# Kernel tuning notes

Hardware: AMD Instinct MI355X
Metric: run time of the kernel (lower is better)

## Reference

```python
import jax, jax.numpy as jnp
import numpy as np

B, S, HID, NH = 2, 2048, 1024, 16
HD = HID // NH  # head_dim = 64


def setup_inputs() -> dict:
    key = jax.random.key(0)
    ks = jax.random.split(key, 9)
    init = 0.02
    return {
        "x": jax.random.normal(ks[0], (B, S, HID), dtype=jnp.float32),
        "Wq": jax.random.normal(ks[1], (HID, HID), dtype=jnp.float32) * init,
        "bq": jnp.zeros((HID,), dtype=jnp.float32),
        "Wk": jax.random.normal(ks[2], (HID, HID), dtype=jnp.float32) * init,
        "bk": jnp.zeros((HID,), dtype=jnp.float32),
        "Wv": jax.random.normal(ks[3], (HID, HID), dtype=jnp.float32) * init,
        "bv": jnp.zeros((HID,), dtype=jnp.float32),
        "Wo": jax.random.normal(ks[4], (HID, HID), dtype=jnp.float32) * init,
        "bo": jnp.zeros((HID,), dtype=jnp.float32),
    }


def _split_heads(t):
    # [B, S, HID] -> [B, NH, S, HD]
    return t.reshape(B, S, NH, HD).transpose(0, 2, 1, 3)


def reference(x, Wq, bq, Wk, bk, Wv, bv, Wo, bo):
    q = _split_heads(x @ Wq.T + bq)
    k = _split_heads(x @ Wk.T + bk)
    v = _split_heads(x @ Wv.T + bv)

    # Faithful to source: scores = QK^T / (head_dim ** -0.5) == QK^T * sqrt(head_dim)
    inv_scale = jnp.asarray(HD ** (-0.5), dtype=x.dtype)
    scores = jnp.einsum("bhqd,bhkd->bhqk", q, k) / inv_scale

    causal_mask = jnp.triu(jnp.ones((S, S), dtype=bool), k=1)  # True above diagonal
    scores = jnp.where(causal_mask, jnp.asarray(-jnp.inf, dtype=scores.dtype), scores)
    attn = jax.nn.softmax(scores, axis=-1)  # dropout = identity (eval mode)

    ctx = jnp.einsum("bhqk,bhkd->bhqd", attn, v)
    ctx = ctx.transpose(0, 2, 1, 3).reshape(B, S, HID)
    out = ctx @ Wo.T + bo  # out_layer Linear; dropout = identity
    return out, attn
```

## Files before the change

### kernel.cpp

```cpp
#include <hip/hip_runtime.h>
#include <hip/hip_bf16.h>

#define BB   2
#define SS   2048
#define HID  1024
#define NH   16
#define HD   64
#define NEGS -30000.0f

typedef __bf16 bf16x8 __attribute__((ext_vector_type(8)));
typedef float  f32x4  __attribute__((ext_vector_type(4)));

static __device__ __forceinline__ f32x4 mfma_bf16(bf16x8 a, bf16x8 b, f32x4 c) {
    return __builtin_amdgcn_mfma_f32_16x16x32_bf16(a, b, c, 0, 0, 0);
}

static __device__ __forceinline__ void split_bf16(float f, __bf16* hp, __bf16* lp) {
    __bf16 h = (__bf16)f;
    *hp = h;
    *lp = (__bf16)(f - (float)h);
}

static __device__ __forceinline__ float clampf(float v, float lo, float hi) {
    return fminf(fmaxf(v, lo), hi);
}

__global__ __launch_bounds__(256) void qkv_kernel(
    const float* __restrict__ x,
    const float* __restrict__ Wq, const float* __restrict__ bq,
    const float* __restrict__ Wk, const float* __restrict__ bk,
    const float* __restrict__ Wv, const float* __restrict__ bv,
    __bf16* __restrict__ qh, __bf16* __restrict__ ql,
    __bf16* __restrict__ kh, __bf16* __restrict__ kl,
    __bf16* __restrict__ vt)
{
    __shared__ __align__(16) __bf16 Ash[64][40], Asl[64][40];
    __shared__ __align__(16) __bf16 Bsh[64][40], Bsl[64][40];
    __shared__ __align__(16) __bf16 Vts[64][72];

    const int nt = blockIdx.x;
    const int mt = blockIdx.y;
    const int stream_id = nt >> 4;
    const int h  = nt & 15;
    const int o0 = h * 64;
    const float* W  = stream_id == 0 ? Wq : (stream_id == 1 ? Wk : Wv);
    const float* bi = stream_id == 0 ? bq : (stream_id == 1 ? bk : bv);

    const int tid  = threadIdx.x;
    const int wave = tid >> 6, lane = tid & 63;
    const int l16  = lane & 15, quad = lane >> 4;

    const f32x4 zero4 = {0.f, 0.f, 0.f, 0.f};
    f32x4 acc[4] = {zero4, zero4, zero4, zero4};

    const int arow = tid >> 2, ac4 = tid & 3;
    const size_t xoff = (size_t)(mt * 64 + arow) * HID + ac4 * 8;
    const size_t woff = (size_t)(o0 + arow) * HID + ac4 * 8;

    for (int k0 = 0; k0 < HID; k0 += 32) {
        __syncthreads();
        float4 a0 = *(const float4*)&x[xoff + k0];
        float4 a1 = *(const float4*)&x[xoff + k0 + 4];
        float4 b0 = *(const float4*)&W[woff + k0];
        float4 b1 = *(const float4*)&W[woff + k0 + 4];
        const float* pa0 = (const float*)&a0;
        const float* pa1 = (const float*)&a1;
        const float* pb0 = (const float*)&b0;
        const float* pb1 = (const float*)&b1;
#pragma unroll
        for (int j = 0; j < 4; j++) {
            split_bf16(pa0[j], &Ash[arow][ac4*8 + j],     &Asl[arow][ac4*8 + j]);
            split_bf16(pa1[j], &Ash[arow][ac4*8 + 4 + j], &Asl[arow][ac4*8 + 4 + j]);
            split_bf16(pb0[j], &Bsh[arow][ac4*8 + j],     &Bsl[arow][ac4*8 + j]);
            split_bf16(pb1[j], &Bsh[arow][ac4*8 + 4 + j], &Bsl[arow][ac4*8 + 4 + j]);
        }
        __syncthreads();
        bf16x8 aH = *(const bf16x8*)&Ash[wave * 16 + l16][quad * 8];
        bf16x8 aL = *(const bf16x8*)&Asl[wave * 16 + l16][quad * 8];
#pragma unroll
        for (int c = 0; c < 4; c++) {
            bf16x8 bH = *(const bf16x8*)&Bsh[c * 16 + l16][quad * 8];
            acc[c] = mfma_bf16(aH, bH, acc[c]);
            if (stream_id < 2) {
                bf16x8 bL = *(const bf16x8*)&Bsl[c * 16 + l16][quad * 8];
                acc[c] = mfma_bf16(aH, bL, acc[c]);
                acc[c] = mfma_bf16(aL, bH, acc[c]);
            }
        }
    }

    const int t0 = mt * 64;
    const int bidx = t0 >> 11;
    const int s0 = t0 & (SS - 1);

    if (stream_id < 2) {
        __bf16* hi_arr = stream_id == 0 ? qh : kh;
        __bf16* lo_arr = stream_id == 0 ? ql : kl;
        const float scale = stream_id == 0 ? 8.0f : 1.0f;
#pragma unroll
        for (int c = 0; c < 4; c++) {
            const int d = c * 16 + l16;
            const float bias = bi[o0 + d];
#pragma unroll
            for (int r = 0; r < 4; r++) {
                const int srow = s0 + wave * 16 + quad * 4 + r;
                float v = clampf((acc[c][r] + bias) * scale, -1e4f, 1e4f);
                __bf16 hv, lv;
                split_bf16(v, &hv, &lv);
                const size_t o = ((size_t)(bidx * NH + h) * SS + srow) * HD + d;
                hi_arr[o] = hv;
                lo_arr[o] = lv;
            }
        }
    } else {
#pragma unroll
        for (int c = 0; c < 4; c++) {
            const int d = c * 16 + l16;
            const float bias = bi[o0 + d];
#pragma unroll
            for (int r = 0; r < 4; r++)
                Vts[d][wave * 16 + quad * 4 + r] =
                    (__bf16)clampf(acc[c][r] + bias, -1e4f, 1e4f);
        }
        __syncthreads();
#pragma unroll
        for (int i = 0; i < 2; i++) {
            const int idx = tid + i * 256;
            const int d = idx >> 3, c8 = idx & 7;
            const size_t o = ((size_t)(bidx * NH + h) * HD + d) * SS + s0 + c8 * 8;
            *(uint4*)&vt[o] = *(const uint4*)&Vts[d][c8 * 8];
        }
    }
}

__global__ __launch_bounds__(256) void attn_kernel(
    const __bf16* __restrict__ qh, const __bf16* __restrict__ ql,
    const __bf16* __restrict__ kh, const __bf16* __restrict__ kl,
    const __bf16* __restrict__ vt,
    float* __restrict__ attn, __bf16* __restrict__ ctx)
{
    __shared__ __align__(16) __bf16 Qh[64][72], Ql[64][72];
    __shared__ __align__(16) __bf16 Kh[64][72], Kl[64][72];
    __shared__ __align__(16) __bf16 Vt[64][72], Ps[64][72];

    const int bid = blockIdx.x;
    const int bh = bid >> 5;
    const int qt = bid & 31;
    const int b = bh >> 4, h = bh & 15;

    const int tid  = threadIdx.x;
    const int wave = tid >> 6, lane = tid & 63;
    const int l16  = lane & 15, quad = lane >> 4;

    {
        const size_t base = ((size_t)bh * SS + qt * 64) * HD;
#pragma unroll
        for (int i = 0; i < 2; i++) {
            const int idx = tid + i * 256;
            const int row = idx >> 3, c8 = idx & 7;
            *(uint4*)&Qh[row][c8 * 8] = *(const uint4*)&qh[base + row * HD + c8 * 8];
            *(uint4*)&Ql[row][c8 * 8] = *(const uint4*)&ql[base + row * HD + c8 * 8];
        }
    }

    float m4[4], l4[4];
#pragma unroll
    for (int r = 0; r < 4; r++) { m4[r] = NEGS; l4[r] = 0.f; }

    const f32x4 zero4 = {0.f, 0.f, 0.f, 0.f};

    for (int kt = 0; kt <= qt; kt++) {
        __syncthreads();
        const size_t base = ((size_t)bh * SS + kt * 64) * HD;
#pragma unroll
        for (int i = 0; i < 2; i++) {
            const int idx = tid + i * 256;
            const int row = idx >> 3, c8 = idx & 7;
            *(uint4*)&Kh[row][c8 * 8] = *(const uint4*)&kh[base + row * HD + c8 * 8];
            *(uint4*)&Kl[row][c8 * 8] = *(const uint4*)&kl[base + row * HD + c8 * 8];
        }
        __syncthreads();

        f32x4 sacc[4] = {zero4, zero4, zero4, zero4};
#pragma unroll
        for (int ks = 0; ks < 2; ks++) {
            bf16x8 aH = *(const bf16x8*)&Qh[wave * 16 + l16][ks * 32 + quad * 8];
            bf16x8 aL = *(const bf16x8*)&Ql[wave * 16 + l16][ks * 32 + quad * 8];
#pragma unroll
            for (int c = 0; c < 4; c++) {
                bf16x8 bH = *(const bf16x8*)&Kh[c * 16 + l16][ks * 32 + quad * 8];
                bf16x8 bL = *(const bf16x8*)&Kl[c * 16 + l16][ks * 32 + quad * 8];
                sacc[c] = mfma_bf16(aH, bH, sacc[c]);
                sacc[c] = mfma_bf16(aH, bL, sacc[c]);
                sacc[c] = mfma_bf16(aL, bH, sacc[c]);
            }
        }
        if (kt == qt) {
#pragma unroll
            for (int c = 0; c < 4; c++) {
                const int col = c * 16 + l16;
#pragma unroll
                for (int r = 0; r < 4; r++)
                    if (col > wave * 16 + quad * 4 + r) sacc[c][r] = NEGS;
            }
        }
#pragma unroll
        for (int r = 0; r < 4; r++) {
            float mx = fmaxf(fmaxf(sacc[0][r], sacc[1][r]), fmaxf(sacc[2][r], sacc[3][r]));
#pragma unroll
            for (int off = 1; off < 16; off <<= 1) mx = fmaxf(mx, __shfl_xor(mx, off));
            const float mn = fmaxf(m4[r], mx);
            float se = __expf(sacc[0][r] - mn) + __expf(sacc[1][r] - mn)
                     + __expf(sacc[2][r] - mn) + __expf(sacc[3][r] - mn);
#pragma unroll
            for (int off = 1; off < 16; off <<= 1) se += __shfl_xor(se, off);
            l4[r] = l4[r] * __expf(m4[r] - mn) + se;
            m4[r] = mn;
        }
    }

    float il[4];
#pragma unroll
    for (int r = 0; r < 4; r++) il[r] = (l4[r] > 0.f) ? (1.0f / l4[r]) : 0.f;

    f32x4 cacc[4] = {zero4, zero4, zero4, zero4};

    for (int kt = 0; kt <= qt; kt++) {
        __syncthreads();
        const size_t kbase = ((size_t)bh * SS + kt * 64) * HD;
        const size_t vbase = (size_t)bh * HD * SS + kt * 64;
#pragma unroll
        for (int i = 0; i < 2; i++) {
            const int idx = tid + i * 256;
            const int row = idx >> 3, c8 = idx & 7;
            *(uint4*)&Kh[row][c8 * 8] = *(const uint4*)&kh[kbase + row * HD + c8 * 8];
            *(uint4*)&Kl[row][c8 * 8] = *(const uint4*)&kl[kbase + row * HD + c8 * 8];
            *(uint4*)&Vt[row][c8 * 8] = *(const uint4*)&vt[vbase + (size_t)row * SS + c8 * 8];
        }
        __syncthreads();

        f32x4 sacc[4] = {zero4, zero4, zero4, zero4};
#pragma unroll
        for (int ks = 0; ks < 2; ks++) {
            bf16x8 aH = *(const bf16x8*)&Qh[wave * 16 + l16][ks * 32 + quad * 8];
            bf16x8 aL = *(const bf16x8*)&Ql[wave * 16 + l16][ks * 32 + quad * 8];
#pragma unroll
            for (int c = 0; c < 4; c++) {
                bf16x8 bH = *(const bf16x8*)&Kh[c * 16 + l16][ks * 32 + quad * 8];
                bf16x8 bL = *(const bf16x8*)&Kl[c * 16 + l16][ks * 32 + quad * 8];
                sacc[c] = mfma_bf16(aH, bH, sacc[c]);
                sacc[c] = mfma_bf16(aH, bL, sacc[c]);
                sacc[c] = mfma_bf16(aL, bH, sacc[c]);
            }
        }
        if (kt == qt) {
#pragma unroll
            for (int c = 0; c < 4; c++) {
                const int col = c * 16 + l16;
#pragma unroll
                for (int r = 0; r < 4; r++)
                    if (col > wave * 16 + quad * 4 + r) sacc[c][r] = NEGS;
            }
        }
#pragma unroll
        for (int c = 0; c < 4; c++) {
#pragma unroll
            for (int r = 0; r < 4; r++) {
                float p = clampf(__expf(sacc[c][r] - m4[r]) * il[r], 0.f, 1.f);
                Ps[wave * 16 + quad * 4 + r][c * 16 + l16] = (__bf16)p;
            }
        }
        __syncthreads();
#pragma unroll
        for (int i = 0; i < 2; i++) {
            const int idx = tid + i * 256;
            const int row = idx >> 3, c8 = idx & 7;
            const size_t o = ((size_t)bh * SS + qt * 64 + row) * SS + kt * 64 + c8 * 8;
            __bf16 tmp[8];
            *(uint4*)tmp = *(const uint4*)&Ps[row][c8 * 8];
            float4 f0, f1;
            f0.x = (float)tmp[0]; f0.y = (float)tmp[1];
            f0.z = (float)tmp[2]; f0.w = (float)tmp[3];
            f1.x = (float)tmp[4]; f1.y = (float)tmp[5];
            f1.z = (float)tmp[6]; f1.w = (float)tmp[7];
            *(float4*)&attn[o]     = f0;
            *(float4*)&attn[o + 4] = f1;
        }
#pragma unroll
        for (int ks = 0; ks < 2; ks++) {
            bf16x8 ap = *(const bf16x8*)&Ps[wave * 16 + l16][ks * 32 + quad * 8];
#pragma unroll
            for (int dt = 0; dt < 4; dt++) {
                bf16x8 bv8 = *(const bf16x8*)&Vt[dt * 16 + l16][ks * 32 + quad * 8];
                cacc[dt] = mfma_bf16(ap, bv8, cacc[dt]);
            }
        }
    }

    const float4 zf4 = {0.f, 0.f, 0.f, 0.f};
    for (int kt = qt + 1; kt < SS / 64; kt++) {
#pragma unroll
        for (int i = 0; i < 4; i++) {
            const int idx = tid + i * 256;
            const int row = idx >> 4, c4 = idx & 15;
            const size_t o = ((size_t)bh * SS + qt * 64 + row) * SS + kt * 64 + c4 * 4;
            *(float4*)&attn[o] = zf4;
        }
    }

#pragma unroll
    for (int dt = 0; dt < 4; dt++) {
        const int d = dt * 16 + l16;
#pragma unroll
        for (int r = 0; r < 4; r++) {
            const int srow = qt * 64 + wave * 16 + quad * 4 + r;
            ctx[(size_t)(b * SS + srow) * HID + h * 64 + d] =
                (__bf16)clampf(cacc[dt][r], -1e4f, 1e4f);
        }
    }
}

__global__ __launch_bounds__(256) void out_kernel(
    const __bf16* __restrict__ ctx, const float* __restrict__ Wo,
    const float* __restrict__ bo, float* __restrict__ out)
{
    __shared__ __align__(16) __bf16 As[64][40];
    __shared__ __align__(16) __bf16 Bs[64][40];

    const int nt = blockIdx.x;
    const int mt = blockIdx.y;
    const int o0 = nt * 64;

    const int tid  = threadIdx.x;
    const int wave = tid >> 6, lane = tid & 63;
    const int l16  = lane & 15, quad = lane >> 4;

    const f32x4 zero4 = {0.f, 0.f, 0.f, 0.f};
    f32x4 acc[4] = {zero4, zero4, zero4, zero4};

    const int arow = tid >> 2, ac4 = tid & 3;
    const size_t aoff = (size_t)(mt * 64 + arow) * HID + ac4 * 8;
    const size_t woff = (size_t)(o0 + arow) * HID + ac4 * 8;

    for (int k0 = 0; k0 < HID; k0 += 32) {
        __syncthreads();
        *(uint4*)&As[arow][ac4 * 8] = *(const uint4*)&ctx[aoff + k0];
        float4 b0 = *(const float4*)&Wo[woff + k0];
        float4 b1 = *(const float4*)&Wo[woff + k0 + 4];
        const float* pb0 = (const float*)&b0;
        const float* pb1 = (const float*)&b1;
#pragma unroll
        for (int j = 0; j < 4; j++) {
            Bs[arow][ac4 * 8 + j]     = (__bf16)pb0[j];
            Bs[arow][ac4 * 8 + 4 + j] = (__bf16)pb1[j];
        }
        __syncthreads();
        bf16x8 a = *(const bf16x8*)&As[wave * 16 + l16][quad * 8];
#pragma unroll
        for (int c = 0; c < 4; c++) {
            bf16x8 b = *(const bf16x8*)&Bs[c * 16 + l16][quad * 8];
            acc[c] = mfma_bf16(a, b, acc[c]);
        }
    }

#pragma unroll
    for (int c = 0; c < 4; c++) {
        const int d = o0 + c * 16 + l16;
        const float bias = bo[d];
#pragma unroll
        for (int r = 0; r < 4; r++) {
            const int t = mt * 64 + wave * 16 + quad * 4 + r;
            out[(size_t)t * HID + d] = clampf(acc[c][r] + bias, -1e4f, 1e4f);
        }
    }
}

extern "C" void kernel_launch(void* const* d_in, const int* in_sizes, int n_in,
                              void* d_out, int out_size, void* d_ws, size_t ws_size,
                              hipStream_t stream) {
    const float* x  = (const float*)d_in[0];
    const float* Wq = (const float*)d_in[1];
    const float* bq = (const float*)d_in[2];
    const float* Wk = (const float*)d_in[3];
    const float* bk = (const float*)d_in[4];
    const float* Wv = (const float*)d_in[5];
    const float* bv = (const float*)d_in[6];
    const float* Wo = (const float*)d_in[7];
    const float* bo = (const float*)d_in[8];

    float* out  = (float*)d_out;
    float* attn = out + (size_t)BB * SS * HID;

    const size_t NQ = (size_t)BB * NH * SS * HD;
    __bf16* ws  = (__bf16*)d_ws;
    __bf16* qh  = ws;
    __bf16* ql  = qh + NQ;
    __bf16* kh  = ql + NQ;
    __bf16* kl  = kh + NQ;
    __bf16* vt  = kl + NQ;
    __bf16* ctx = vt + NQ;

    qkv_kernel<<<dim3(48, 64), 256, 0, stream>>>(x, Wq, bq, Wk, bk, Wv, bv,
                                                 qh, ql, kh, kl, vt);
    attn_kernel<<<dim3(1024), 256, 0, stream>>>(qh, ql, kh, kl, vt, attn, ctx);
    out_kernel<<<dim3(16, 64), 256, 0, stream>>>(ctx, Wo, bo, out);
}
```

Before: 890.5 us.

## Presplit Q/K weights, fuse QKV tiles, single-pass attention with stored raw scores

A new pre-kernel splits Wq and Wk into bf16 hi/lo arrays once, so the QKV kernel loads them directly. The QKV kernel now computes a 64x128 tile of Q, K and V together, reusing the split x tile across all three. Attention changes from two passes (statistics, then recompute) to one online-softmax pass that writes raw scores to the attn output and rescales them in a second read-modify-write sweep. Query tiles are scheduled heaviest-first. The QKV kernel now holds many accumulators, which raises register pressure, and the extra global round trip over attn adds memory traffic.

```diff
diff --git a/kernel.cpp b/kernel.cpp
--- a/kernel.cpp
+++ b/kernel.cpp
@@ -25,111 +25,161 @@
     return fminf(fmaxf(v, lo), hi);
 }
 
+__global__ __launch_bounds__(256) void wsplit_kernel(
+    const float* __restrict__ Wq, const float* __restrict__ Wk,
+    __bf16* __restrict__ wqh, __bf16* __restrict__ wql,
+    __bf16* __restrict__ wkh, __bf16* __restrict__ wkl)
+{
+    const size_t o = ((size_t)blockIdx.x * 256 + threadIdx.x) * 4;
+    float4 q = *(const float4*)&Wq[o];
+    float4 k = *(const float4*)&Wk[o];
+    __bf16 qhv[4], qlv[4], khv[4], klv[4];
+    split_bf16(q.x, &qhv[0], &qlv[0]); split_bf16(q.y, &qhv[1], &qlv[1]);
+    split_bf16(q.z, &qhv[2], &qlv[2]); split_bf16(q.w, &qhv[3], &qlv[3]);
+    split_bf16(k.x, &khv[0], &klv[0]); split_bf16(k.y, &khv[1], &klv[1]);
+    split_bf16(k.z, &khv[2], &klv[2]); split_bf16(k.w, &khv[3], &klv[3]);
+    *(uint2*)&wqh[o] = *(uint2*)qhv;
+    *(uint2*)&wql[o] = *(uint2*)qlv;
+    *(uint2*)&wkh[o] = *(uint2*)khv;
+    *(uint2*)&wkl[o] = *(uint2*)klv;
+}
+
+#define AH_O   0
+#define AL_O   2560
+#define BQH_O  5120
+#define BQL_O  10240
+#define BKH_O  15360
+#define BKL_O  20480
+#define BVH_O  25600
+
 __global__ __launch_bounds__(256) void qkv_kernel(
     const float* __restrict__ x,
-    const float* __restrict__ Wq, const float* __restrict__ bq,
-    const float* __restrict__ Wk, const float* __restrict__ bk,
-    const float* __restrict__ Wv, const float* __restrict__ bv,
+    const __bf16* __restrict__ wqh, const __bf16* __restrict__ wql,
+    const __bf16* __restrict__ wkh, const __bf16* __restrict__ wkl,
+    const float* __restrict__ Wv,
+    const float* __restrict__ bq, const float* __restrict__ bk,
+    const float* __restrict__ bv,
     __bf16* __restrict__ qh, __bf16* __restrict__ ql,
     __bf16* __restrict__ kh, __bf16* __restrict__ kl,
     __bf16* __restrict__ vt)
 {
-    __shared__ __align__(16) __bf16 Ash[64][40], Asl[64][40];
-    __shared__ __align__(16) __bf16 Bsh[64][40], Bsl[64][40];
-    __shared__ __align__(16) __bf16 Vts[64][72];
-
-    const int nt = blockIdx.x;
+    __shared__ __align__(16) __bf16 SM[30720];
+
+    const int hp = blockIdx.x;
     const int mt = blockIdx.y;
-    const int stream_id = nt >> 4;
-    const int h  = nt & 15;
-    const int o0 = h * 64;
-    const float* W  = stream_id == 0 ? Wq : (stream_id == 1 ? Wk : Wv);
-    const float* bi = stream_id == 0 ? bq : (stream_id == 1 ? bk : bv);
+    const int o0 = hp * 128;
 
     const int tid  = threadIdx.x;
     const int wave = tid >> 6, lane = tid & 63;
     const int l16  = lane & 15, quad = lane >> 4;
 
     const f32x4 zero4 = {0.f, 0.f, 0.f, 0.f};
-    f32x4 acc[4] = {zero4, zero4, zero4, zero4};
+    f32x4 aq[8], ak[8], av[8];
+#pragma unroll
+    for (int c = 0; c < 8; c++) { aq[c] = zero4; ak[c] = zero4; av[c] = zero4; }
 
     const int arow = tid >> 2, ac4 = tid & 3;
     const size_t xoff = (size_t)(mt * 64 + arow) * HID + ac4 * 8;
-    const size_t woff = (size_t)(o0 + arow) * HID + ac4 * 8;
 
     for (int k0 = 0; k0 < HID; k0 += 32) {
         __syncthreads();
-        float4 a0 = *(const float4*)&x[xoff + k0];
-        float4 a1 = *(const float4*)&x[xoff + k0 + 4];
-        float4 b0 = *(const float4*)&W[woff + k0];
-        float4 b1 = *(const float4*)&W[woff + k0 + 4];
-        const float* pa0 = (const float*)&a0;
-        const float* pa1 = (const float*)&a1;
-        const float* pb0 = (const float*)&b0;
-        const float* pb1 = (const float*)&b1;
-#pragma unroll
-        for (int j = 0; j < 4; j++) {
-            split_bf16(pa0[j], &Ash[arow][ac4*8 + j],     &Asl[arow][ac4*8 + j]);
-            split_bf16(pa1[j], &Ash[arow][ac4*8 + 4 + j], &Asl[arow][ac4*8 + 4 + j]);
-            split_bf16(pb0[j], &Bsh[arow][ac4*8 + j],     &Bsl[arow][ac4*8 + j]);
-            split_bf16(pb1[j], &Bsh[arow][ac4*8 + 4 + j], &Bsl[arow][ac4*8 + 4 + j]);
-        }
-        __syncthreads();
-        bf16x8 aH = *(const bf16x8*)&Ash[wave * 16 + l16][quad * 8];
-        bf16x8 aL = *(const bf16x8*)&Asl[wave * 16 + l16][quad * 8];
-#pragma unroll
-        for (int c = 0; c < 4; c++) {
-            bf16x8 bH = *(const bf16x8*)&Bsh[c * 16 + l16][quad * 8];
-            acc[c] = mfma_bf16(aH, bH, acc[c]);
-            if (stream_id < 2) {
-                bf16x8 bL = *(const bf16x8*)&Bsl[c * 16 + l16][quad * 8];
-                acc[c] = mfma_bf16(aH, bL, acc[c]);
-                acc[c] = mfma_bf16(aL, bH, acc[c]);
-            }
+        {
+            float4 a0 = *(const float4*)&x[xoff + k0];
+            float4 a1 = *(const float4*)&x[xoff + k0 + 4];
+            __bf16 hh[8], ll[8];
+            split_bf16(a0.x, &hh[0], &ll[0]); split_bf16(a0.y, &hh[1], &ll[1]);
+            split_bf16(a0.z, &hh[2], &ll[2]); split_bf16(a0.w, &hh[3], &ll[3]);
+            split_bf16(a1.x, &hh[4], &ll[4]); split_bf16(a1.y, &hh[5], &ll[5]);
+            split_bf16(a1.z, &hh[6], &ll[6]); split_bf16(a1.w, &hh[7], &ll[7]);
+            const int ldst = arow * 40 + ac4 * 8;
+            *(uint4*)&SM[AH_O + ldst] = *(uint4*)hh;
+            *(uint4*)&SM[AL_O + ldst] = *(uint4*)ll;
+        }
+#pragma unroll
+        for (int j = 0; j < 2; j++) {
+            const int bidx = tid + j * 256;
+            const int brow = bidx >> 2, bc4 = bidx & 3;
+            const size_t so = (size_t)(o0 + brow) * HID + k0 + bc4 * 8;
+            const int ldst = brow * 40 + bc4 * 8;
+            *(uint4*)&SM[BQH_O + ldst] = *(const uint4*)&wqh[so];
+            *(uint4*)&SM[BQL_O + ldst] = *(const uint4*)&wql[so];
+            *(uint4*)&SM[BKH_O + ldst] = *(const uint4*)&wkh[so];
+            *(uint4*)&SM[BKL_O + ldst] = *(const uint4*)&wkl[so];
+            float4 v0 = *(const float4*)&Wv[so];
+            float4 v1 = *(const float4*)&Wv[so + 4];
+            __bf16 vh[8];
+            vh[0] = (__bf16)v0.x; vh[1] = (__bf16)v0.y;
+            vh[2] = (__bf16)v0.z; vh[3] = (__bf16)v0.w;
+            vh[4] = (__bf16)v1.x; vh[5] = (__bf16)v1.y;
+            vh[6] = (__bf16)v1.z; vh[7] = (__bf16)v1.w;
+            *(uint4*)&SM[BVH_O + ldst] = *(uint4*)vh;
+        }
+        __syncthreads();
+
+        const int aoff = (wave * 16 + l16) * 40 + quad * 8;
+        bf16x8 aH = *(const bf16x8*)&SM[AH_O + aoff];
+        bf16x8 aL = *(const bf16x8*)&SM[AL_O + aoff];
+#pragma unroll
+        for (int c = 0; c < 8; c++) {
+            const int boff = (c * 16 + l16) * 40 + quad * 8;
+            bf16x8 bH = *(const bf16x8*)&SM[BQH_O + boff];
+            bf16x8 bL = *(const bf16x8*)&SM[BQL_O + boff];
+            aq[c] = mfma_bf16(aH, bH, aq[c]);
+            aq[c] = mfma_bf16(aH, bL, aq[c]);
+            aq[c] = mfma_bf16(aL, bH, aq[c]);
+            bH = *(const bf16x8*)&SM[BKH_O + boff];
+            bL = *(const bf16x8*)&SM[BKL_O + boff];
+            ak[c] = mfma_bf16(aH, bH, ak[c]);
+            ak[c] = mfma_bf16(aH, bL, ak[c]);
+            ak[c] = mfma_bf16(aL, bH, ak[c]);
+            bH = *(const bf16x8*)&SM[BVH_O + boff];
+            av[c] = mfma_bf16(aH, bH, av[c]);
         }
     }
 
     const int t0 = mt * 64;
-    const int bidx = t0 >> 11;
+    const int bb = t0 >> 11;
     const int s0 = t0 & (SS - 1);
 
-    if (stream_id < 2) {
-        __bf16* hi_arr = stream_id == 0 ? qh : kh;
-        __bf16* lo_arr = stream_id == 0 ? ql : kl;
-        const float scale = stream_id == 0 ? 8.0f : 1.0f;
-#pragma unroll
-        for (int c = 0; c < 4; c++) {
-            const int d = c * 16 + l16;
-            const float bias = bi[o0 + d];
-#pragma unroll
-            for (int r = 0; r < 4; r++) {
-                const int srow = s0 + wave * 16 + quad * 4 + r;
-                float v = clampf((acc[c][r] + bias) * scale, -1e4f, 1e4f);
-                __bf16 hv, lv;
-                split_bf16(v, &hv, &lv);
-                const size_t o = ((size_t)(bidx * NH + h) * SS + srow) * HD + d;
-                hi_arr[o] = hv;
-                lo_arr[o] = lv;
-            }
-        }
-    } else {
-#pragma unroll
-        for (int c = 0; c < 4; c++) {
-            const int d = c * 16 + l16;
-            const float bias = bi[o0 + d];
-#pragma unroll
-            for (int r = 0; r < 4; r++)
-                Vts[d][wave * 16 + quad * 4 + r] =
-                    (__bf16)clampf(acc[c][r] + bias, -1e4f, 1e4f);
-        }
-        __syncthreads();
-#pragma unroll
-        for (int i = 0; i < 2; i++) {
-            const int idx = tid + i * 256;
-            const int d = idx >> 3, c8 = idx & 7;
-            const size_t o = ((size_t)(bidx * NH + h) * HD + d) * SS + s0 + c8 * 8;
-            *(uint4*)&vt[o] = *(const uint4*)&Vts[d][c8 * 8];
-        }
+#pragma unroll
+    for (int c = 0; c < 8; c++) {
+        const int og   = o0 + c * 16 + l16;
+        const int head = og >> 6;
+        const int d    = og & 63;
+        const float bqv = bq[og];
+        const float bkv = bk[og];
+#pragma unroll
+        for (int r = 0; r < 4; r++) {
+            const int srow = s0 + wave * 16 + quad * 4 + r;
+            const size_t o = ((size_t)(bb * NH + head) * SS + srow) * HD + d;
+            float vq = clampf((aq[c][r] + bqv) * 8.0f, -1e4f, 1e4f);
+            __bf16 hv, lv;
+            split_bf16(vq, &hv, &lv);
+            qh[o] = hv; ql[o] = lv;
+            float vk = clampf(ak[c][r] + bkv, -1e4f, 1e4f);
+            split_bf16(vk, &hv, &lv);
+            kh[o] = hv; kl[o] = lv;
+        }
+    }
+
+    __syncthreads();
+#pragma unroll
+    for (int c = 0; c < 8; c++) {
+        const int col = c * 16 + l16;
+        const float bvv = bv[o0 + col];
+#pragma unroll
+        for (int r = 0; r < 4; r++)
+            SM[col * 72 + wave * 16 + quad * 4 + r] =
+                (__bf16)clampf(av[c][r] + bvv, -1e4f, 1e4f);
+    }
+    __syncthreads();
+#pragma unroll
+    for (int i = 0; i < 4; i++) {
+        const int idx = tid + i * 256;
+        const int col = idx >> 3, c8 = idx & 7;
+        const int head = col >> 6, d = col & 63;
+        const size_t o = ((size_t)(bb * NH + hp * 2 + head) * HD + d) * SS + s0 + c8 * 8;
+        *(uint4*)&vt[o] = *(const uint4*)&SM[col * 72 + c8 * 8];
     }
 }
 
@@ -142,10 +192,11 @@
     __shared__ __align__(16) __bf16 Qh[64][72], Ql[64][72];
     __shared__ __align__(16) __bf16 Kh[64][72], Kl[64][72];
     __shared__ __align__(16) __bf16 Vt[64][72], Ps[64][72];
+    __shared__ float m_sh[64], il_sh[64];
 
     const int bid = blockIdx.x;
-    const int bh = bid >> 5;
-    const int qt = bid & 31;
+    const int qt = 31 - (bid >> 5);
+    const int bh = bid & 31;
     const int b = bh >> 4, h = bh & 15;
 
     const int tid  = threadIdx.x;
@@ -165,19 +216,24 @@
 
     float m4[4], l4[4];
 #pragma unroll
-    for (int r = 0; r < 4; r++) { m4[r] = NEGS; l4[r] = 0.f; }
+    for (int r = 0; r < 4; r++) { m4[r] = -1e30f; l4[r] = 0.f; }
 
     const f32x4 zero4 = {0.f, 0.f, 0.f, 0.f};
+    f32x4 cacc[4] = {zero4, zero4, zero4, zero4};
+
+    const size_t srow_base = (size_t)bh * SS + qt * 64;
 
     for (int kt = 0; kt <= qt; kt++) {
         __syncthreads();
-        const size_t base = ((size_t)bh * SS + kt * 64) * HD;
+        const size_t kbase = ((size_t)bh * SS + kt * 64) * HD;
+        const size_t vbase = (size_t)bh * HD * SS + kt * 64;
 #pragma unroll
         for (int i = 0; i < 2; i++) {
             const int idx = tid + i * 256;
             const int row = idx >> 3, c8 = idx & 7;
-            *(uint4*)&Kh[row][c8 * 8] = *(const uint4*)&kh[base + row * HD + c8 * 8];
-            *(uint4*)&Kl[row][c8 * 8] = *(const uint4*)&kl[base + row * HD + c8 * 8];
+            *(uint4*)&Kh[row][c8 * 8] = *(const uint4*)&kh[kbase + row * HD + c8 * 8];
+            *(uint4*)&Kl[row][c8 * 8] = *(const uint4*)&kl[kbase + row * HD + c8 * 8];
+            *(uint4*)&Vt[row][c8 * 8] = *(const uint4*)&vt[vbase + (size_t)row * SS + c8 * 8];
         }
         __syncthreads();
 
@@ -205,86 +261,37 @@
             }
         }
 #pragma unroll
+        for (int c = 0; c < 4; c++) {
+#pragma unroll
+            for (int r = 0; r < 4; r++) {
+                const size_t o = (srow_base + wave * 16 + quad * 4 + r) * SS
+                               + kt * 64 + c * 16 + l16;
+                attn[o] = sacc[c][r];
+            }
+        }
+#pragma unroll
         for (int r = 0; r < 4; r++) {
             float mx = fmaxf(fmaxf(sacc[0][r], sacc[1][r]), fmaxf(sacc[2][r], sacc[3][r]));
 #pragma unroll
             for (int off = 1; off < 16; off <<= 1) mx = fmaxf(mx, __shfl_xor(mx, off));
             const float mn = fmaxf(m4[r], mx);
-            float se = __expf(sacc[0][r] - mn) + __expf(sacc[1][r] - mn)
-                     + __expf(sacc[2][r] - mn) + __expf(sacc[3][r] - mn);
+            const float p0 = __expf(sacc[0][r] - mn);
+            const float p1 = __expf(sacc[1][r] - mn);
+            const float p2 = __expf(sacc[2][r] - mn);
+            const float p3 = __expf(sacc[3][r] - mn);
+            float se = p0 + p1 + p2 + p3;
 #pragma unroll
             for (int off = 1; off < 16; off <<= 1) se += __shfl_xor(se, off);
-            l4[r] = l4[r] * __expf(m4[r] - mn) + se;
+            const float alpha = __expf(m4[r] - mn);
+            l4[r] = l4[r] * alpha + se;
             m4[r] = mn;
-        }
-    }
-
-    float il[4];
-#pragma unroll
-    for (int r = 0; r < 4; r++) il[r] = (l4[r] > 0.f) ? (1.0f / l4[r]) : 0.f;
-
-    f32x4 cacc[4] = {zero4, zero4, zero4, zero4};
-
-    for (int kt = 0; kt <= qt; kt++) {
-        __syncthreads();
-        const size_t kbase = ((size_t)bh * SS + kt * 64) * HD;
-        const size_t vbase = (size_t)bh * HD * SS + kt * 64;
-#pragma unroll
-        for (int i = 0; i < 2; i++) {
-            const int idx = tid + i * 256;
-            const int row = idx >> 3, c8 = idx & 7;
-            *(uint4*)&Kh[row][c8 * 8] = *(const uint4*)&kh[kbase + row * HD + c8 * 8];
-            *(uint4*)&Kl[row][c8 * 8] = *(const uint4*)&kl[kbase + row * HD + c8 * 8];
-            *(uint4*)&Vt[row][c8 * 8] = *(const uint4*)&vt[vbase + (size_t)row * SS + c8 * 8];
-        }
-        __syncthreads();
-
-        f32x4 sacc[4] = {zero4, zero4, zero4, zero4};
-#pragma unroll
-        for (int ks = 0; ks < 2; ks++) {
-            bf16x8 aH = *(const bf16x8*)&Qh[wave * 16 + l16][ks * 32 + quad * 8];
-            bf16x8 aL = *(const bf16x8*)&Ql[wave * 16 + l16][ks * 32 + quad * 8];
-#pragma unroll
-            for (int c = 0; c < 4; c++) {
-                bf16x8 bH = *(const bf16x8*)&Kh[c * 16 + l16][ks * 32 + quad * 8];
-                bf16x8 bL = *(const bf16x8*)&Kl[c * 16 + l16][ks * 32 + quad * 8];
-                sacc[c] = mfma_bf16(aH, bH, sacc[c]);
-                sacc[c] = mfma_bf16(aH, bL, sacc[c]);
-                sacc[c] = mfma_bf16(aL, bH, sacc[c]);
-            }
-        }
-        if (kt == qt) {
-#pragma unroll
-            for (int c = 0; c < 4; c++) {
-                const int col = c * 16 + l16;
-#pragma unroll
-                for (int r = 0; r < 4; r++)
-                    if (col > wave * 16 + quad * 4 + r) sacc[c][r] = NEGS;
-            }
-        }
-#pragma unroll
-        for (int c = 0; c < 4; c++) {
-#pragma unroll
-            for (int r = 0; r < 4; r++) {
-                float p = clampf(__expf(sacc[c][r] - m4[r]) * il[r], 0.f, 1.f);
-                Ps[wave * 16 + quad * 4 + r][c * 16 + l16] = (__bf16)p;
-            }
-        }
-        __syncthreads();
-#pragma unroll
-        for (int i = 0; i < 2; i++) {
-            const int idx = tid + i * 256;
-            const int row = idx >> 3, c8 = idx & 7;
-            const size_t o = ((size_t)bh * SS + qt * 64 + row) * SS + kt * 64 + c8 * 8;
-            __bf16 tmp[8];
-            *(uint4*)tmp = *(const uint4*)&Ps[row][c8 * 8];
-            float4 f0, f1;
-            f0.x = (float)tmp[0]; f0.y = (float)tmp[1];
-            f0.z = (float)tmp[2]; f0.w = (float)tmp[3];
-            f1.x = (float)tmp[4]; f1.y = (float)tmp[5];
-            f1.z = (float)tmp[6]; f1.w = (float)tmp[7];
-            *(float4*)&attn[o]     = f0;
-            *(float4*)&attn[o + 4] = f1;
+#pragma unroll
+            for (int dt = 0; dt < 4; dt++) cacc[dt][r] *= alpha;
+            const int rr = wave * 16 + quad * 4 + r;
+            Ps[rr][l16]      = (__bf16)p0;
+            Ps[rr][16 + l16] = (__bf16)p1;
+            Ps[rr][32 + l16] = (__bf16)p2;
+            Ps[rr][48 + l16] = (__bf16)p3;
         }
 #pragma unroll
         for (int ks = 0; ks < 2; ks++) {
@@ -297,13 +304,40 @@
         }
     }
 
-    const float4 zf4 = {0.f, 0.f, 0.f, 0.f};
-    for (int kt = qt + 1; kt < SS / 64; kt++) {
+    float il[4];
+#pragma unroll
+    for (int r = 0; r < 4; r++) il[r] = (l4[r] > 0.f) ? (1.0f / l4[r]) : 0.f;
+    if (l16 == 0) {
+#pragma unroll
+        for (int r = 0; r < 4; r++) {
+            m_sh[wave * 16 + quad * 4 + r]  = m4[r];
+            il_sh[wave * 16 + quad * 4 + r] = il[r];
+        }
+    }
+    __syncthreads();
+
+    for (int kt = 0; kt <= qt; kt++) {
 #pragma unroll
         for (int i = 0; i < 4; i++) {
             const int idx = tid + i * 256;
             const int row = idx >> 4, c4 = idx & 15;
-            const size_t o = ((size_t)bh * SS + qt * 64 + row) * SS + kt * 64 + c4 * 4;
+            const size_t o = (srow_base + row) * SS + kt * 64 + c4 * 4;
+            float4 v = *(const float4*)&attn[o];
+            const float mm = m_sh[row], ii = il_sh[row];
+            v.x = __expf(v.x - mm) * ii;
+            v.y = __expf(v.y - mm) * ii;
+            v.z = __expf(v.z - mm) * ii;
+            v.w = __expf(v.w - mm) * ii;
+            *(float4*)&attn[o] = v;
+        }
+    }
+    const float4 zf4 = {0.f, 0.f, 0.f, 0.f};
+    for (int kt = qt + 1; kt < SS / 64; kt++) {
+#pragma unroll
+        for (int i = 0; i < 4; i++) {
+            const int idx = tid + i * 256;
+            const int row = idx >> 4, c4 = idx & 15;
+            const size_t o = (srow_base + row) * SS + kt * 64 + c4 * 4;
             *(float4*)&attn[o] = zf4;
         }
     }
@@ -315,7 +349,7 @@
         for (int r = 0; r < 4; r++) {
             const int srow = qt * 64 + wave * 16 + quad * 4 + r;
             ctx[(size_t)(b * SS + srow) * HID + h * 64 + d] =
-                (__bf16)clampf(cacc[dt][r], -1e4f, 1e4f);
+                (__bf16)clampf(cacc[dt][r] * il[r], -1e4f, 1e4f);
         }
     }
 }
@@ -347,13 +381,12 @@
         *(uint4*)&As[arow][ac4 * 8] = *(const uint4*)&ctx[aoff + k0];
         float4 b0 = *(const float4*)&Wo[woff + k0];
         float4 b1 = *(const float4*)&Wo[woff + k0 + 4];
-        const float* pb0 = (const float*)&b0;
-        const float* pb1 = (const float*)&b1;
-#pragma unroll
-        for (int j = 0; j < 4; j++) {
-            Bs[arow][ac4 * 8 + j]     = (__bf16)pb0[j];
-            Bs[arow][ac4 * 8 + 4 + j] = (__bf16)pb1[j];
-        }
+        __bf16 bh8[8];
+        bh8[0] = (__bf16)b0.x; bh8[1] = (__bf16)b0.y;
+        bh8[2] = (__bf16)b0.z; bh8[3] = (__bf16)b0.w;
+        bh8[4] = (__bf16)b1.x; bh8[5] = (__bf16)b1.y;
+        bh8[6] = (__bf16)b1.z; bh8[7] = (__bf16)b1.w;
+        *(uint4*)&Bs[arow][ac4 * 8] = *(uint4*)bh8;
         __syncthreads();
         bf16x8 a = *(const bf16x8*)&As[wave * 16 + l16][quad * 8];
 #pragma unroll
@@ -392,16 +425,22 @@
     float* attn = out + (size_t)BB * SS * HID;
 
     const size_t NQ = (size_t)BB * NH * SS * HD;
+    const size_t NW = (size_t)HID * HID;
     __bf16* ws  = (__bf16*)d_ws;
     __bf16* qh  = ws;
     __bf16* ql  = qh + NQ;
     __bf16* kh  = ql + NQ;
     __bf16* kl  = kh + NQ;
     __bf16* vt  = kl + NQ;
-    __bf16* ctx = vt + NQ;
-
-    qkv_kernel<<<dim3(48, 64), 256, 0, stream>>>(x, Wq, bq, Wk, bk, Wv, bv,
-                                                 qh, ql, kh, kl, vt);
+    __bf16* wqh = vt + NQ;
+    __bf16* wql = wqh + NW;
+    __bf16* wkh = wql + NW;
+    __bf16* wkl = wkh + NW;
+    __bf16* ctx = wqh;
+
+    wsplit_kernel<<<dim3(1024), 256, 0, stream>>>(Wq, Wk, wqh, wql, wkh, wkl);
+    qkv_kernel<<<dim3(8, 64), 256, 0, stream>>>(x, wqh, wql, wkh, wkl, Wv,
+                                                bq, bk, bv, qh, ql, kh, kl, vt);
     attn_kernel<<<dim3(1024), 256, 0, stream>>>(qh, ql, kh, kl, vt, attn, ctx);
     out_kernel<<<dim3(16, 64), 256, 0, stream>>>(ctx, Wo, bo, out);
 }
```

Result: slower. 968.6 us (+8.8%).
